# Optimization experiments

Measured on AMD Instinct MI355X. Metric: run time of the kernel, lower is better.

## Reference

```python
import jax, jax.numpy as jnp
import numpy as np

N, F, U = 32768, 512, 512
GRID_SIZE, SPLINE_ORDER = 3, 3
GRID_RANGE = (-1.0, 1.0)
LN_EPS = 1e-3  # keras LayerNormalization default epsilon


def _make_grid():
    h = (GRID_RANGE[1] - GRID_RANGE[0]) / GRID_SIZE
    start = -SPLINE_ORDER * h + GRID_RANGE[0]
    stop = (GRID_SIZE + SPLINE_ORDER) * h + GRID_RANGE[0]
    num = GRID_SIZE + 2 * SPLINE_ORDER + 1  # 10 knots
    g = np.linspace(start, stop, num, dtype=np.float32)
    g = np.tile(g, (F, 1))[None, :, :]  # [1, F, num]
    return jnp.asarray(g)


def _glorot(key, shape):
    limit = np.sqrt(6.0 / (shape[0] + shape[1])).astype(np.float32)
    return jax.random.uniform(key, shape, jnp.float32, -limit, limit)


def setup_inputs() -> dict:
    key = jax.random.key(0)
    k_x, k_bw, k_sw = jax.random.split(key, 3)
    return {
        "x": jax.random.normal(k_x, (N, F), jnp.float32),
        "ln_gamma": jnp.ones((F,), jnp.float32),
        "ln_beta": jnp.zeros((F,), jnp.float32),
        "base_weight": _glorot(k_bw, (F, U)),
        "base_bias": jnp.zeros((U,), jnp.float32),
        "spline_weight": _glorot(k_sw, (F * (GRID_SIZE + SPLINE_ORDER), U)),
        "grid": _make_grid(),
    }


def _b_splines(x, grid):
    # x: [N, F]; grid: [1, F, G+2K+1]
    xe = x[..., None]  # [N, F, 1]
    bases = ((xe >= grid[..., :-1]) & (xe < grid[..., 1:])).astype(x.dtype)  # [N,F,G+2K]
    for k in range(1, SPLINE_ORDER + 1):
        left = (xe - grid[..., :-(k + 1)]) / (grid[..., k:-1] - grid[..., :-(k + 1)])
        right = (grid[..., k + 1:] - xe) / (grid[..., k + 1:] - grid[..., 1:-k])
        bases = left * bases[..., :-1] + right * bases[..., 1:]
    return bases.reshape(x.shape[0], -1)  # [N, F*(G+K)]


def reference(x, ln_gamma, ln_beta, base_weight, base_bias, spline_weight, grid):
    # LayerNorm over last axis
    mean = jnp.mean(x, axis=-1, keepdims=True)
    var = jnp.var(x, axis=-1, keepdims=True)
    xn = (x - mean) * jax.lax.rsqrt(var + LN_EPS) * ln_gamma + ln_beta
    # base branch: relu -> matmul -> bias
    base_out = jax.nn.relu(xn) @ base_weight + base_bias
    # spline branch: Cox-de Boor basis -> matmul
    spline_out = _b_splines(xn, grid) @ spline_weight
    # dropout rate 0 / inference -> identity
    return base_out + spline_out
```

## Files before the change

### kernel.cpp

```cpp
#include <hip/hip_runtime.h>
#include <hip/hip_bf16.h>


#define N_ROWS 32768
#define F_DIM  512
#define U_DIM  512
#define K_DIM  4096

typedef short short8 __attribute__((ext_vector_type(8)));
typedef float floatx4 __attribute__((ext_vector_type(4)));

__device__ __forceinline__ float bf2f(unsigned short h) {
    return __uint_as_float(((unsigned int)h) << 16);
}
__device__ __forceinline__ bool probe_bf16(const void* grid) {
    return ((const unsigned int*)grid)[0] != 0xC0400000u;
}
template <bool B16>
__device__ __forceinline__ float ldf(const void* p, int i) {
    return B16 ? bf2f(((const unsigned short*)p)[i]) : ((const float*)p)[i];
}
template <bool B16>
__device__ __forceinline__ void ld2(const void* p, int i, float* o) {
    if (B16) {
        ushort2 v = *(const ushort2*)((const unsigned short*)p + i);
        o[0] = bf2f(v.x); o[1] = bf2f(v.y);
    } else {
        float2 v = *(const float2*)((const float*)p + i);
        o[0] = v.x; o[1] = v.y;
    }
}
template <bool B16>
__device__ __forceinline__ void ld4(const void* p, int i, float* o) {
    if (B16) {
        ushort4 v = *(const ushort4*)((const unsigned short*)p + i);
        o[0] = bf2f(v.x); o[1] = bf2f(v.y); o[2] = bf2f(v.z); o[3] = bf2f(v.w);
    } else {
        float4 v = *(const float4*)((const float*)p + i);
        o[0] = v.x; o[1] = v.y; o[2] = v.z; o[3] = v.w;
    }
}
__device__ __forceinline__ unsigned int pk2(float lo, float hi) {
    __hip_bfloat162 h = __float22bfloat162_rn(make_float2(lo, hi));
    return *reinterpret_cast<unsigned int*>(&h);
}

template <bool B16>
__device__ __forceinline__ void ln_stats_body(const void* __restrict__ x,
                                              float2* __restrict__ stats) {
    int wave = threadIdx.x >> 6, lane = threadIdx.x & 63;
    int row = blockIdx.x * 4 + wave;
    float v[8];
    ld4<B16>(x, row * F_DIM + lane * 8, v);
    ld4<B16>(x, row * F_DIM + lane * 8 + 4, v + 4);
    float s = 0.f, s2 = 0.f;
#pragma unroll
    for (int k = 0; k < 8; ++k) { s += v[k]; s2 += v[k] * v[k]; }
#pragma unroll
    for (int off = 32; off > 0; off >>= 1) {
        s  += __shfl_xor(s, off);
        s2 += __shfl_xor(s2, off);
    }
    if (lane == 0) {
        float mean = s * (1.0f / F_DIM);
        float var  = s2 * (1.0f / F_DIM) - mean * mean;
        stats[row] = make_float2(mean, rsqrtf(var + 1e-3f));
    }
}
__global__ __launch_bounds__(256) void ln_stats_k(const void* __restrict__ x,
                                                  const void* __restrict__ grid,
                                                  float2* __restrict__ stats) {
    if (probe_bf16(grid)) ln_stats_body<true>(x, stats);
    else                  ln_stats_body<false>(x, stats);
}

template <bool B16>
__device__ __forceinline__ void build_wt_body(const void* __restrict__ bw,
                                              const void* __restrict__ sw,
                                              unsigned short* __restrict__ wt) {
    int idx = blockIdx.x * 256 + threadIdx.x;
    int u = idx & 511;
    int fq = idx >> 9;
#pragma unroll
    for (int i = 0; i < 4; ++i) {
        int f = fq * 4 + i;
        uint4 w;
        w.x = pk2(ldf<B16>(bw, f * U_DIM + u),            ldf<B16>(sw, (f * 6 + 0) * U_DIM + u));
        w.y = pk2(ldf<B16>(sw, (f * 6 + 1) * U_DIM + u),  ldf<B16>(sw, (f * 6 + 2) * U_DIM + u));
        w.z = pk2(ldf<B16>(sw, (f * 6 + 3) * U_DIM + u),  ldf<B16>(sw, (f * 6 + 4) * U_DIM + u));
        w.w = pk2(ldf<B16>(sw, (f * 6 + 5) * U_DIM + u),  0.f);
        *(uint4*)(wt + (size_t)u * K_DIM + f * 8) = w;
    }
}
__global__ __launch_bounds__(256) void build_wt_k(const void* __restrict__ bw,
                                                  const void* __restrict__ sw,
                                                  const void* __restrict__ grid,
                                                  unsigned short* __restrict__ wt) {
    if (probe_bf16(grid)) build_wt_body<true>(bw, sw, wt);
    else                  build_wt_body<false>(bw, sw, wt);
}

template <bool B16>
__device__ __forceinline__ void kan_gemm_body(
    const void* __restrict__ x,
    const float2* __restrict__ stats,
    const unsigned short* __restrict__ wt,
    const void* __restrict__ gam,
    const void* __restrict__ bet,
    const void* __restrict__ bias,
    void* __restrict__ out) {
    __shared__ __align__(16) unsigned short Alds[128 * 32];
    __shared__ __align__(16) unsigned short Blds[256 * 32];

    const int tid = threadIdx.x;
    const int lane = tid & 63, wv = tid >> 6;
    const int ctile = blockIdx.x;
    const int rtile = blockIdx.y;

    const int arow = tid & 127, fg = tid >> 7;
    const int grow = rtile * 128 + arow;
    float2 st = stats[grow];
    const float mean = st.x, rstd = st.y;
    const int xoff = grow * F_DIM + fg * 2;
    const int goff = fg * 2;
    const int aslot0 = ((arow >> 4) * 4 + fg * 2) * 16 + (arow & 15);
    uint4* aptr0 = (uint4*)&Alds[aslot0 * 8];
    uint4* aptr1 = (uint4*)&Alds[(aslot0 + 16) * 8];

    const unsigned short* gsrc[4];
    unsigned short* ldst[4];
#pragma unroll
    for (int i = 0; i < 4; ++i) {
        int s = wv * 256 + i * 64 + lane;
        int C = ((s >> 6) << 4) | (s & 15);
        int q = (s >> 4) & 3;
        gsrc[i] = wt + (size_t)(ctile * 256 + C) * K_DIM + q * 8;
        ldst[i] = &Blds[(wv * 256 + i * 64) * 8];
    }

    const int wr = wv >> 1, wc = wv & 1;
    const int lr = lane & 15, lq = lane >> 4;

    floatx4 acc[4][8];
#pragma unroll
    for (int mi = 0; mi < 4; ++mi)
#pragma unroll
        for (int ni = 0; ni < 8; ++ni) acc[mi][ni] = (floatx4){0.f, 0.f, 0.f, 0.f};

    for (int ks = 0; ks < K_DIM / 32; ++ks) {
#pragma unroll
        for (int i = 0; i < 4; ++i)
            __builtin_amdgcn_global_load_lds(
                (const __attribute__((address_space(1))) void*)(gsrc[i] + ks * 32),
                (__attribute__((address_space(3))) void*)ldst[i], 16, 0, 0);

        float xs[2], gs[2], bs[2];
        ld2<B16>(x, xoff + ks * 4, xs);
        ld2<B16>(gam, goff + ks * 4, gs);
        ld2<B16>(bet, goff + ks * 4, bs);
        uint4 pkv[2];
#pragma unroll
        for (int i = 0; i < 2; ++i) {
            float xn = fmaf(xs[i] - mean, rstd * gs[i], bs[i]);
            float tt = fmaf(xn, 1.5f, 4.5f);
            float bb[6];
#pragma unroll
            for (int j = 0; j < 6; ++j) {
                float d = tt - (float)(j + 2);
                float a = fabsf(d);
                float a2 = d * d;
                float v1 = fmaf(fmaf(0.5f, a, -1.0f), a2, 0.66666669f);
                float c = fmaxf(2.0f - a, 0.0f);
                float v2 = c * c * c * (1.0f / 6.0f);
                bb[j] = (a < 1.0f) ? v1 : v2;
            }
            pkv[i].x = pk2(fmaxf(xn, 0.f), bb[0]);
            pkv[i].y = pk2(bb[1], bb[2]);
            pkv[i].z = pk2(bb[3], bb[4]);
            pkv[i].w = pk2(bb[5], 0.f);
        }
        *aptr0 = pkv[0];
        *aptr1 = pkv[1];
        __syncthreads();

        short8 afr[4], bfr[8];
#pragma unroll
        for (int mi = 0; mi < 4; ++mi)
            afr[mi] = *(const short8*)&Alds[((wr * 4 + mi) * 64 + lane) * 8];
#pragma unroll
        for (int ni = 0; ni < 8; ++ni)
            bfr[ni] = *(const short8*)&Blds[((wc * 8 + ni) * 64 + lane) * 8];
#pragma unroll
        for (int mi = 0; mi < 4; ++mi)
#pragma unroll
            for (int ni = 0; ni < 8; ++ni)
                acc[mi][ni] = __builtin_amdgcn_mfma_f32_16x16x32_bf16(
                    afr[mi], bfr[ni], acc[mi][ni], 0, 0, 0);
        __syncthreads();
    }

    float biasv[8];
#pragma unroll
    for (int ni = 0; ni < 8; ++ni)
        biasv[ni] = ldf<B16>(bias, ctile * 256 + wc * 128 + ni * 16 + lr);
#pragma unroll
    for (int mi = 0; mi < 4; ++mi)
#pragma unroll
        for (int ni = 0; ni < 8; ++ni)
#pragma unroll
            for (int r = 0; r < 4; ++r) {
                int row = rtile * 128 + wr * 64 + mi * 16 + lq * 4 + r;
                int col = ctile * 256 + wc * 128 + ni * 16 + lr;
                float val = acc[mi][ni][r] + biasv[ni];
                if (B16) ((unsigned short*)out)[(size_t)row * U_DIM + col] =
                    (unsigned short)(pk2(val, 0.f) & 0xffffu);
                else ((float*)out)[(size_t)row * U_DIM + col] = val;
            }
}
__global__ __launch_bounds__(256, 2) void kan_gemm(
    const void* __restrict__ x, const float2* __restrict__ stats,
    const unsigned short* __restrict__ wt, const void* __restrict__ gam,
    const void* __restrict__ bet, const void* __restrict__ bias,
    const void* __restrict__ grid, void* __restrict__ out) {
    if (probe_bf16(grid)) kan_gemm_body<true>(x, stats, wt, gam, bet, bias, out);
    else                  kan_gemm_body<false>(x, stats, wt, gam, bet, bias, out);
}

extern "C" void kernel_launch(void* const* d_in, const int* in_sizes, int n_in,
                              void* d_out, int out_size, void* d_ws, size_t ws_size,
                              hipStream_t stream) {
    const void* x    = d_in[0];
    const void* gam  = d_in[1];
    const void* bet  = d_in[2];
    const void* bw   = d_in[3];
    const void* bb   = d_in[4];
    const void* sw   = d_in[5];
    const void* grid = d_in[6];

    float2* stats = (float2*)d_ws;
    unsigned short* wt = (unsigned short*)((char*)d_ws + N_ROWS * sizeof(float2));

    hipLaunchKernelGGL(ln_stats_k, dim3(N_ROWS / 4), dim3(256), 0, stream, x, grid, stats);
    hipLaunchKernelGGL(build_wt_k, dim3(U_DIM * 128 / 256), dim3(256), 0, stream,
                       bw, sw, grid, wt);
    hipLaunchKernelGGL(kan_gemm, dim3(2, N_ROWS / 128), dim3(256), 0, stream,
                       x, stats, wt, gam, bet, bb, grid, d_out);
}
```

Measured before the change: 312.4 us.

## Pre-tile weights into LDS-ready blocks and retile GEMM to 64x256 with BK=64

The weight-repack kernel now writes the combined weight matrix already in the per-step LDS fragment order, so the GEMM streams contiguous 16-byte chunks. The GEMM tile changes from 128x256 to 64x256 with a K step of 64, halving the barrier count per K. Each wave now owns 64 columns across all 64 rows, and occupancy is raised to 3 blocks per SM. The cost is that each block computes its A basis values for only 64 rows, so B reuse per block drops and more B traffic is loaded per output.

```diff
diff --git a/kernel.cpp b/kernel.cpp
--- a/kernel.cpp
+++ b/kernel.cpp
@@ -6,6 +6,8 @@
 #define F_DIM  512
 #define U_DIM  512
 #define K_DIM  4096
+#define BK     64
+#define NSTEP  (K_DIM / BK)
 
 typedef short short8 __attribute__((ext_vector_type(8)));
 typedef float floatx4 __attribute__((ext_vector_type(4)));
@@ -77,91 +79,80 @@
 template <bool B16>
 __device__ __forceinline__ void build_wt_body(const void* __restrict__ bw,
                                               const void* __restrict__ sw,
-                                              unsigned short* __restrict__ wt) {
-    int idx = blockIdx.x * 256 + threadIdx.x;
-    int u = idx & 511;
-    int fq = idx >> 9;
-#pragma unroll
-    for (int i = 0; i < 4; ++i) {
-        int f = fq * 4 + i;
-        uint4 w;
-        w.x = pk2(ldf<B16>(bw, f * U_DIM + u),            ldf<B16>(sw, (f * 6 + 0) * U_DIM + u));
-        w.y = pk2(ldf<B16>(sw, (f * 6 + 1) * U_DIM + u),  ldf<B16>(sw, (f * 6 + 2) * U_DIM + u));
-        w.z = pk2(ldf<B16>(sw, (f * 6 + 3) * U_DIM + u),  ldf<B16>(sw, (f * 6 + 4) * U_DIM + u));
-        w.w = pk2(ldf<B16>(sw, (f * 6 + 5) * U_DIM + u),  0.f);
-        *(uint4*)(wt + (size_t)u * K_DIM + f * 8) = w;
-    }
+                                              unsigned short* __restrict__ wt2) {
+    int chunk = blockIdx.x * 256 + threadIdx.x;
+    int ct   = chunk >> 17;
+    int ks   = (chunk >> 11) & 63;
+    int slot = chunk & 2047;
+    int C = ((slot >> 7) << 4) | (slot & 15);
+    int q = (slot >> 4) & 7;
+    int u = ct * 256 + C;
+    int f = ks * 8 + q;
+    uint4 w;
+    w.x = pk2(ldf<B16>(bw, f * U_DIM + u),           ldf<B16>(sw, (f * 6 + 0) * U_DIM + u));
+    w.y = pk2(ldf<B16>(sw, (f * 6 + 1) * U_DIM + u), ldf<B16>(sw, (f * 6 + 2) * U_DIM + u));
+    w.z = pk2(ldf<B16>(sw, (f * 6 + 3) * U_DIM + u), ldf<B16>(sw, (f * 6 + 4) * U_DIM + u));
+    w.w = pk2(ldf<B16>(sw, (f * 6 + 5) * U_DIM + u), 0.f);
+    ((uint4*)wt2)[chunk] = w;
 }
 __global__ __launch_bounds__(256) void build_wt_k(const void* __restrict__ bw,
                                                   const void* __restrict__ sw,
                                                   const void* __restrict__ grid,
-                                                  unsigned short* __restrict__ wt) {
-    if (probe_bf16(grid)) build_wt_body<true>(bw, sw, wt);
-    else                  build_wt_body<false>(bw, sw, wt);
+                                                  unsigned short* __restrict__ wt2) {
+    if (probe_bf16(grid)) build_wt_body<true>(bw, sw, wt2);
+    else                  build_wt_body<false>(bw, sw, wt2);
 }
 
 template <bool B16>
 __device__ __forceinline__ void kan_gemm_body(
     const void* __restrict__ x,
     const float2* __restrict__ stats,
-    const unsigned short* __restrict__ wt,
+    const unsigned short* __restrict__ wt2,
     const void* __restrict__ gam,
     const void* __restrict__ bet,
     const void* __restrict__ bias,
     void* __restrict__ out) {
-    __shared__ __align__(16) unsigned short Alds[128 * 32];
-    __shared__ __align__(16) unsigned short Blds[256 * 32];
+    __shared__ __align__(16) unsigned short Alds[512 * 8];
+    __shared__ __align__(16) unsigned short Blds[2048 * 8];
 
     const int tid = threadIdx.x;
     const int lane = tid & 63, wv = tid >> 6;
-    const int ctile = blockIdx.x;
-    const int rtile = blockIdx.y;
-
-    const int arow = tid & 127, fg = tid >> 7;
-    const int grow = rtile * 128 + arow;
+    const int rt = blockIdx.x;
+    const int ct = blockIdx.y;
+
+    const int r = tid & 63, h = tid >> 6;
+    const int grow = rt * 64 + r;
     float2 st = stats[grow];
     const float mean = st.x, rstd = st.y;
-    const int xoff = grow * F_DIM + fg * 2;
-    const int goff = fg * 2;
-    const int aslot0 = ((arow >> 4) * 4 + fg * 2) * 16 + (arow & 15);
-    uint4* aptr0 = (uint4*)&Alds[aslot0 * 8];
-    uint4* aptr1 = (uint4*)&Alds[(aslot0 + 16) * 8];
-
-    const unsigned short* gsrc[4];
-    unsigned short* ldst[4];
-#pragma unroll
-    for (int i = 0; i < 4; ++i) {
-        int s = wv * 256 + i * 64 + lane;
-        int C = ((s >> 6) << 4) | (s & 15);
-        int q = (s >> 4) & 3;
-        gsrc[i] = wt + (size_t)(ctile * 256 + C) * K_DIM + q * 8;
-        ldst[i] = &Blds[(wv * 256 + i * 64) * 8];
-    }
-
-    const int wr = wv >> 1, wc = wv & 1;
-    const int lr = lane & 15, lq = lane >> 4;
-
-    floatx4 acc[4][8];
+    const int xoff = grow * F_DIM + h * 2;
+    const int goff = h * 2;
+    unsigned short* aw = &Alds[(((r >> 4) * 8 + h * 2) * 16 + (r & 15)) * 8];
+
+    const unsigned short* bsrc0 =
+        wt2 + ((size_t)ct * 64 * 2048 + wv * 512 + lane) * 8;
+    unsigned short* bdst0 = &Blds[wv * 512 * 8];
+
+    floatx4 acc[4][4];
 #pragma unroll
     for (int mi = 0; mi < 4; ++mi)
 #pragma unroll
-        for (int ni = 0; ni < 8; ++ni) acc[mi][ni] = (floatx4){0.f, 0.f, 0.f, 0.f};
-
-    for (int ks = 0; ks < K_DIM / 32; ++ks) {
-#pragma unroll
-        for (int i = 0; i < 4; ++i)
+        for (int ni = 0; ni < 4; ++ni) acc[mi][ni] = (floatx4){0.f, 0.f, 0.f, 0.f};
+
+    for (int ks = 0; ks < NSTEP; ++ks) {
+        const unsigned short* bs = bsrc0 + (size_t)ks * 2048 * 8;
+#pragma unroll
+        for (int i = 0; i < 8; ++i)
             __builtin_amdgcn_global_load_lds(
-                (const __attribute__((address_space(1))) void*)(gsrc[i] + ks * 32),
-                (__attribute__((address_space(3))) void*)ldst[i], 16, 0, 0);
-
-        float xs[2], gs[2], bs[2];
-        ld2<B16>(x, xoff + ks * 4, xs);
-        ld2<B16>(gam, goff + ks * 4, gs);
-        ld2<B16>(bet, goff + ks * 4, bs);
-        uint4 pkv[2];
+                (const __attribute__((address_space(1))) void*)(bs + i * 512),
+                (__attribute__((address_space(3))) void*)(bdst0 + i * 512), 16, 0, 0);
+
+        float xs[2], gs[2], bs2[2];
+        ld2<B16>(x, xoff + ks * 8, xs);
+        ld2<B16>(gam, goff + ks * 8, gs);
+        ld2<B16>(bet, goff + ks * 8, bs2);
 #pragma unroll
         for (int i = 0; i < 2; ++i) {
-            float xn = fmaf(xs[i] - mean, rstd * gs[i], bs[i]);
+            float xn = fmaf(xs[i] - mean, rstd * gs[i], bs2[i]);
             float tt = fmaf(xn, 1.5f, 4.5f);
             float bb[6];
 #pragma unroll
@@ -174,56 +165,61 @@
                 float v2 = c * c * c * (1.0f / 6.0f);
                 bb[j] = (a < 1.0f) ? v1 : v2;
             }
-            pkv[i].x = pk2(fmaxf(xn, 0.f), bb[0]);
-            pkv[i].y = pk2(bb[1], bb[2]);
-            pkv[i].z = pk2(bb[3], bb[4]);
-            pkv[i].w = pk2(bb[5], 0.f);
+            uint4 pkv;
+            pkv.x = pk2(fmaxf(xn, 0.f), bb[0]);
+            pkv.y = pk2(bb[1], bb[2]);
+            pkv.z = pk2(bb[3], bb[4]);
+            pkv.w = pk2(bb[5], 0.f);
+            *(uint4*)(aw + i * 16 * 8) = pkv;
         }
-        *aptr0 = pkv[0];
-        *aptr1 = pkv[1];
         __syncthreads();
 
-        short8 afr[4], bfr[8];
-#pragma unroll
-        for (int mi = 0; mi < 4; ++mi)
-            afr[mi] = *(const short8*)&Alds[((wr * 4 + mi) * 64 + lane) * 8];
-#pragma unroll
-        for (int ni = 0; ni < 8; ++ni)
-            bfr[ni] = *(const short8*)&Blds[((wc * 8 + ni) * 64 + lane) * 8];
-#pragma unroll
-        for (int mi = 0; mi < 4; ++mi)
-#pragma unroll
-            for (int ni = 0; ni < 8; ++ni)
-                acc[mi][ni] = __builtin_amdgcn_mfma_f32_16x16x32_bf16(
-                    afr[mi], bfr[ni], acc[mi][ni], 0, 0, 0);
+#pragma unroll
+        for (int kk = 0; kk < 2; ++kk) {
+            short8 afr[4], bfr[4];
+#pragma unroll
+            for (int mi = 0; mi < 4; ++mi)
+                afr[mi] = *(const short8*)&Alds[((mi * 8 + kk * 4) * 16) * 8 + lane * 8];
+#pragma unroll
+            for (int ni = 0; ni < 4; ++ni)
+                bfr[ni] = *(const short8*)
+                    &Blds[(((wv * 4 + ni) * 8 + kk * 4) * 16) * 8 + lane * 8];
+#pragma unroll
+            for (int mi = 0; mi < 4; ++mi)
+#pragma unroll
+                for (int ni = 0; ni < 4; ++ni)
+                    acc[mi][ni] = __builtin_amdgcn_mfma_f32_16x16x32_bf16(
+                        afr[mi], bfr[ni], acc[mi][ni], 0, 0, 0);
+        }
         __syncthreads();
     }
 
-    float biasv[8];
-#pragma unroll
-    for (int ni = 0; ni < 8; ++ni)
-        biasv[ni] = ldf<B16>(bias, ctile * 256 + wc * 128 + ni * 16 + lr);
+    const int lr = lane & 15, lq = lane >> 4;
+    float biasv[4];
+#pragma unroll
+    for (int ni = 0; ni < 4; ++ni)
+        biasv[ni] = ldf<B16>(bias, ct * 256 + wv * 64 + ni * 16 + lr);
 #pragma unroll
     for (int mi = 0; mi < 4; ++mi)
 #pragma unroll
-        for (int ni = 0; ni < 8; ++ni)
-#pragma unroll
-            for (int r = 0; r < 4; ++r) {
-                int row = rtile * 128 + wr * 64 + mi * 16 + lq * 4 + r;
-                int col = ctile * 256 + wc * 128 + ni * 16 + lr;
-                float val = acc[mi][ni][r] + biasv[ni];
+        for (int ni = 0; ni < 4; ++ni)
+#pragma unroll
+            for (int rr = 0; rr < 4; ++rr) {
+                int row = rt * 64 + mi * 16 + lq * 4 + rr;
+                int col = ct * 256 + wv * 64 + ni * 16 + lr;
+                float val = acc[mi][ni][rr] + biasv[ni];
                 if (B16) ((unsigned short*)out)[(size_t)row * U_DIM + col] =
                     (unsigned short)(pk2(val, 0.f) & 0xffffu);
                 else ((float*)out)[(size_t)row * U_DIM + col] = val;
             }
 }
-__global__ __launch_bounds__(256, 2) void kan_gemm(
+__global__ __launch_bounds__(256, 3) void kan_gemm(
     const void* __restrict__ x, const float2* __restrict__ stats,
-    const unsigned short* __restrict__ wt, const void* __restrict__ gam,
+    const unsigned short* __restrict__ wt2, const void* __restrict__ gam,
     const void* __restrict__ bet, const void* __restrict__ bias,
     const void* __restrict__ grid, void* __restrict__ out) {
-    if (probe_bf16(grid)) kan_gemm_body<true>(x, stats, wt, gam, bet, bias, out);
-    else                  kan_gemm_body<false>(x, stats, wt, gam, bet, bias, out);
+    if (probe_bf16(grid)) kan_gemm_body<true>(x, stats, wt2, gam, bet, bias, out);
+    else                  kan_gemm_body<false>(x, stats, wt2, gam, bet, bias, out);
 }
 
 extern "C" void kernel_launch(void* const* d_in, const int* in_sizes, int n_in,
@@ -238,11 +234,10 @@
     const void* grid = d_in[6];
 
     float2* stats = (float2*)d_ws;
-    unsigned short* wt = (unsigned short*)((char*)d_ws + N_ROWS * sizeof(float2));
+    unsigned short* wt2 = (unsigned short*)((char*)d_ws + N_ROWS * sizeof(float2));
 
     hipLaunchKernelGGL(ln_stats_k, dim3(N_ROWS / 4), dim3(256), 0, stream, x, grid, stats);
-    hipLaunchKernelGGL(build_wt_k, dim3(U_DIM * 128 / 256), dim3(256), 0, stream,
-                       bw, sw, grid, wt);
-    hipLaunchKernelGGL(kan_gemm, dim3(2, N_ROWS / 128), dim3(256), 0, stream,
-                       x, stats, wt, gam, bet, bb, grid, d_out);
-}
+    hipLaunchKernelGGL(build_wt_k, dim3(1024), dim3(256), 0, stream, bw, sw, grid, wt2);
+    hipLaunchKernelGGL(kan_gemm, dim3(N_ROWS / 64, 2), dim3(256), 0, stream,
+                       x, stats, wt2, gam, bet, bb, grid, d_out);
+}
```

Result: slower. 321.1 us (+2.8%).
